# Optimization experiments

Measured on AMD Instinct MI355X. Metric: run time of the kernel, lower is better.

Reference implementation:

```python
import jax, jax.numpy as jnp
import numpy as np

B, C, H, W, S = 32, 512, 32, 32, 4
HW = H * W
OUT = HW // S  # conv1/conv2 out channels = 256
EPS = 1e-5


def setup_inputs() -> dict:
    key = jax.random.key(0)
    ks = jax.random.split(key, 8)
    d = {}
    d["x"] = jax.random.normal(ks[0], (B, C, H, W), jnp.float32)
    # conv1 / bn1 (operate on x_flat with 'channels' = h*w)
    d["w1"] = jax.random.normal(ks[1], (OUT, HW), jnp.float32) * 0.02
    d["b1"] = jnp.zeros((OUT,), jnp.float32)
    d["g1"] = jnp.ones((OUT,), jnp.float32)
    d["be1"] = jnp.zeros((OUT,), jnp.float32)
    d["m1"] = jax.random.normal(ks[2], (OUT,), jnp.float32) * 0.01
    d["v1"] = jnp.ones((OUT,), jnp.float32)
    # conv2 / bn2
    d["w2"] = jax.random.normal(ks[3], (OUT, HW), jnp.float32) * 0.02
    d["b2"] = jnp.zeros((OUT,), jnp.float32)
    d["g2"] = jnp.ones((OUT,), jnp.float32)
    d["be2"] = jnp.zeros((OUT,), jnp.float32)
    d["m2"] = jax.random.normal(ks[4], (OUT,), jnp.float32) * 0.01
    d["v2"] = jnp.ones((OUT,), jnp.float32)
    # conv3 / bn3 (1x1 conv on the real channel dim c)
    d["w3"] = jax.random.normal(ks[5], (C, C), jnp.float32) * 0.02
    d["b3"] = jnp.zeros((C,), jnp.float32)
    d["g3"] = jnp.ones((C,), jnp.float32)
    d["be3"] = jnp.zeros((C,), jnp.float32)
    d["m3"] = jax.random.normal(ks[6], (C,), jnp.float32) * 0.01
    d["v3"] = jnp.ones((C,), jnp.float32)
    # conv4: 1x1 conv mapping 1+2c channels -> 1
    d["w4"] = jax.random.normal(ks[7], (1 + 2 * C,), jnp.float32) * 0.02
    d["b4"] = jnp.zeros((), jnp.float32)
    return d


def _bn1d(t, g, be, m, v):
    # t: [b, o, c]; BatchNorm (eval mode) over channel axis 1
    scale = g / jnp.sqrt(v + EPS)
    return (t - m[:, None]) * scale[:, None] + be[:, None]


def reference(x, w1, b1, g1, be1, m1, v1,
              w2, b2, g2, be2, m2, v2,
              w3, b3, g3, be3, m3, v3,
              w4, b4):
    b, c, h, w = x.shape
    # x_flat: [b, h*w, c] -- conv1/conv2 are 1x1 convs over 'channels' = h*w
    xf = x.reshape(b, c, h * w).transpose(0, 2, 1)
    theta = jax.nn.relu(_bn1d(jnp.einsum('oq,bqc->boc', w1, xf) + b1[:, None],
                              g1, be1, m1, v1))  # [b, OUT, c]
    phi = jax.nn.relu(_bn1d(jnp.einsum('oq,bqc->boc', w2, xf) + b2[:, None],
                            g2, be2, m2, v2))    # [b, OUT, c]
    # per-batch conv2d-as-matmul loop collapses to one batched GEMM:
    # affinity[b, i, j] = sum_k phi[b, k, i] * theta[b, k, j]
    aff = jnp.einsum('bki,bkj->bij', phi, theta)  # [b, c, c]
    # x_embed: 1x1 conv + BN + ReLU + global average pool -> [b, c]
    scale3 = g3 / jnp.sqrt(v3 + EPS)
    xe = jnp.einsum('oc,bchw->bohw', w3, x) + b3[:, None, None]
    xe = jax.nn.relu((xe - m3[:, None, None]) * scale3[:, None, None]
                     + be3[:, None, None])
    xe = xe.mean(axis=(2, 3))  # [b, c]
    # conv4 over y = cat([x_embed, affinity_a, affinity_b], dim=1):
    # affinity_a[b,i,0,p] = aff[b,i,p]; affinity_b[b,i,0,p] = aff[b,p,i]
    logits = (w4[0] * xe
              + jnp.einsum('i,bip->bp', w4[1:1 + c], aff)
              + jnp.einsum('i,bpi->bp', w4[1 + c:], aff)
              + b4)
    a = jax.nn.sigmoid(logits)  # [b, c]
    return x * a[:, :, None, None]
```

## Files before the change

kernel.cpp:

```cpp
#include <hip/hip_runtime.h>
#include <math.h>

#define BB   32
#define CC   512
#define HWW  1024
#define OUTC 256
#define EPSV 1e-5f

typedef __attribute__((ext_vector_type(8))) short bfrag;
typedef __attribute__((ext_vector_type(4))) float f32x4;

__device__ inline unsigned short f2bf(float x){
  unsigned int uu = __float_as_uint(x);
  uu += 0x7fff + ((uu >> 16) & 1);
  return (unsigned short)(uu >> 16);
}
__device__ inline float bf2f(unsigned short h){
  return __uint_as_float(((unsigned int)h) << 16);
}

#define ASYNC16(g, l) \
  __builtin_amdgcn_global_load_lds((const __attribute__((address_space(1))) unsigned int*)(g), \
                                   (__attribute__((address_space(3))) unsigned int*)(l), 16, 0, 0)


__global__ __launch_bounds__(256) void kw_conv(
    const float* __restrict__ w1, const float* __restrict__ w2,
    const float* __restrict__ w3,
    unsigned short* __restrict__ Whi, unsigned short* __restrict__ Wlo,
    unsigned short* __restrict__ W3hi)
{
  int i = blockIdx.x * 256 + threadIdx.x;
  if (i < 512 * 1024) {
    float v = (i < 256 * 1024) ? w1[i] : w2[i - 256 * 1024];
    unsigned short h = f2bf(v);
    Whi[i] = h;
    Wlo[i] = f2bf(v - bf2f(h));
  } else {
    int j = i - 512 * 1024;
    W3hi[j] = f2bf(w3[j]);
  }
}

__global__ __launch_bounds__(256) void k0_x(
    const float* __restrict__ x,
    unsigned short* __restrict__ Xhi, unsigned short* __restrict__ Xlo,
    unsigned short* __restrict__ XThi)
{
  __shared__ float T[64][65];
  const int b = blockIdx.z, c0 = blockIdx.y * 64, p0 = blockIdx.x * 64;
  const int tid = threadIdx.x, tr = tid >> 4, tc4 = (tid & 15) * 4;
  const float* xb = x + (size_t)b * 512 * 1024;
#pragma unroll
  for (int r = 0; r < 4; ++r) {
    int c = c0 + tr + r * 16;
    float4 v = *(const float4*)(xb + (size_t)c * 1024 + p0 + tc4);
    T[tr + r * 16][tc4 + 0] = v.x; T[tr + r * 16][tc4 + 1] = v.y;
    T[tr + r * 16][tc4 + 2] = v.z; T[tr + r * 16][tc4 + 3] = v.w;
    ushort4 h, l;
    h.x = f2bf(v.x); l.x = f2bf(v.x - bf2f(h.x));
    h.y = f2bf(v.y); l.y = f2bf(v.y - bf2f(h.y));
    h.z = f2bf(v.z); l.z = f2bf(v.z - bf2f(h.z));
    h.w = f2bf(v.w); l.w = f2bf(v.w - bf2f(h.w));
    size_t idx = (size_t)b * 524288 + (size_t)c * 1024 + p0 + tc4;
    *(ushort4*)(Xhi + idx) = h;
    *(ushort4*)(Xlo + idx) = l;
  }
  __syncthreads();
#pragma unroll
  for (int r = 0; r < 4; ++r) {
    int pl = tr + r * 16;
    ushort4 h;
    h.x = f2bf(T[tc4 + 0][pl]); h.y = f2bf(T[tc4 + 1][pl]);
    h.z = f2bf(T[tc4 + 2][pl]); h.w = f2bf(T[tc4 + 3][pl]);
    *(ushort4*)(XThi + (size_t)b * 524288 + (size_t)(p0 + pl) * 512 + c0 + tc4) = h;
  }
}

__global__ __launch_bounds__(256) void g1_mfma(
    const unsigned short* __restrict__ Xhi, const unsigned short* __restrict__ Xlo,
    const unsigned short* __restrict__ Whi, const unsigned short* __restrict__ Wlo,
    const float* __restrict__ b1p, const float* __restrict__ g1p,
    const float* __restrict__ be1p, const float* __restrict__ m1p, const float* __restrict__ v1p,
    const float* __restrict__ b2p, const float* __restrict__ g2p,
    const float* __restrict__ be2p, const float* __restrict__ m2p, const float* __restrict__ v2p,
    float* __restrict__ P2)
{
  __shared__ unsigned short sAh[4096], sAl[4096], sBh[4096], sBl[4096];
  const int b  = blockIdx.z;
  const int n0 = blockIdx.x * 128;
  const int c0 = blockIdx.y * 128;
  const int tid = threadIdx.x;
  const int wave = tid >> 6, lane = tid & 63;
  const int lr = lane >> 2, lc = (lane & 3) * 8;
  const int wm = wave & 1, wn = wave >> 1;
  const int fr = lane & 15, fq = lane >> 4;

  const unsigned short* gb; unsigned short* lb;
  if (wave == 0)      { gb = Xhi + (size_t)b * 524288 + (size_t)c0 * 1024; lb = sAh; }
  else if (wave == 1) { gb = Xlo + (size_t)b * 524288 + (size_t)c0 * 1024; lb = sAl; }
  else if (wave == 2) { gb = Whi + (size_t)n0 * 1024; lb = sBh; }
  else                { gb = Wlo + (size_t)n0 * 1024; lb = sBl; }
  gb += (size_t)lr * 1024 + lc;

  f32x4 acc[4][4];
  const f32x4 zz = {0.f, 0.f, 0.f, 0.f};
#pragma unroll
  for (int i = 0; i < 4; ++i)
#pragma unroll
    for (int j = 0; j < 4; ++j) acc[i][j] = zz;

  for (int kq = 0; kq < 1024; kq += 32) {
#pragma unroll
    for (int inst = 0; inst < 8; ++inst)
      ASYNC16(gb + (size_t)inst * 16 * 1024 + kq, lb + inst * 512);
    __syncthreads();
    bfrag ah[4], al[4], bh[4], bl[4];
#pragma unroll
    for (int i = 0; i < 4; ++i) {
      int off = (wm * 64 + i * 16 + fr) * 32 + fq * 8;
      ah[i] = *(const bfrag*)&sAh[off];
      al[i] = *(const bfrag*)&sAl[off];
    }
#pragma unroll
    for (int j = 0; j < 4; ++j) {
      int off = (wn * 64 + j * 16 + fr) * 32 + fq * 8;
      bh[j] = *(const bfrag*)&sBh[off];
      bl[j] = *(const bfrag*)&sBl[off];
    }
#pragma unroll
    for (int i = 0; i < 4; ++i)
#pragma unroll
      for (int j = 0; j < 4; ++j) {
        acc[i][j] = __builtin_amdgcn_mfma_f32_16x16x32_bf16(ah[i], bh[j], acc[i][j], 0, 0, 0);
        acc[i][j] = __builtin_amdgcn_mfma_f32_16x16x32_bf16(ah[i], bl[j], acc[i][j], 0, 0, 0);
        acc[i][j] = __builtin_amdgcn_mfma_f32_16x16x32_bf16(al[i], bh[j], acc[i][j], 0, 0, 0);
      }
    __syncthreads();
  }

#pragma unroll
  for (int j = 0; j < 4; ++j) {
    int co = n0 + wn * 64 + j * 16 + fr;
    float sc, sh;
    if (co < 256) {
      float s = g1p[co] * rsqrtf(v1p[co] + EPSV);
      sc = s; sh = (b1p[co] - m1p[co]) * s + be1p[co];
    } else {
      int q = co - 256;
      float s = g2p[q] * rsqrtf(v2p[q] + EPSV);
      sc = s; sh = (b2p[q] - m2p[q]) * s + be2p[q];
    }
#pragma unroll
    for (int i = 0; i < 4; ++i) {
      int crow = c0 + wm * 64 + i * 16 + fq * 4;
      float* dst = P2 + ((size_t)b * 512 + crow) * 512 + co;
#pragma unroll
      for (int r = 0; r < 4; ++r)
        dst[(size_t)r * 512] = fmaxf(acc[i][j][r] * sc + sh, 0.f);
    }
  }
}

__global__ __launch_bounds__(256) void g2_mfma(
    const unsigned short* __restrict__ W3hi, const unsigned short* __restrict__ XThi,
    const float* __restrict__ b3p, const float* __restrict__ g3p,
    const float* __restrict__ be3p, const float* __restrict__ m3p, const float* __restrict__ v3p,
    float* __restrict__ xe_acc)
{
  __shared__ unsigned short sA[4096], sB[4096];
  const int b  = blockIdx.z;
  const int n0 = blockIdx.x * 128;
  const int m0 = blockIdx.y * 128;
  const int tid = threadIdx.x;
  const int wave = tid >> 6, lane = tid & 63;
  const int lr = lane >> 2, lc = (lane & 3) * 8;
  const int wm = wave & 1, wn = wave >> 1;
  const int fr = lane & 15, fq = lane >> 4;

  const unsigned short* gb; unsigned short* lb;
  if (wave < 2) { gb = W3hi + (size_t)(m0 + wave * 64) * 512; lb = sA + wave * 2048; }
  else { gb = XThi + (size_t)b * 524288 + (size_t)(n0 + (wave - 2) * 64) * 512; lb = sB + (wave - 2) * 2048; }
  gb += (size_t)lr * 512 + lc;

  f32x4 acc[4][4];
  const f32x4 zz = {0.f, 0.f, 0.f, 0.f};
#pragma unroll
  for (int i = 0; i < 4; ++i)
#pragma unroll
    for (int j = 0; j < 4; ++j) acc[i][j] = zz;

  for (int kq = 0; kq < 512; kq += 32) {
#pragma unroll
    for (int inst = 0; inst < 4; ++inst)
      ASYNC16(gb + (size_t)inst * 16 * 512 + kq, lb + inst * 512);
    __syncthreads();
    bfrag af[4], bf[4];
#pragma unroll
    for (int i = 0; i < 4; ++i)
      af[i] = *(const bfrag*)&sA[(wm * 64 + i * 16 + fr) * 32 + fq * 8];
#pragma unroll
    for (int j = 0; j < 4; ++j)
      bf[j] = *(const bfrag*)&sB[(wn * 64 + j * 16 + fr) * 32 + fq * 8];
#pragma unroll
    for (int i = 0; i < 4; ++i)
#pragma unroll
      for (int j = 0; j < 4; ++j)
        acc[i][j] = __builtin_amdgcn_mfma_f32_16x16x32_bf16(af[i], bf[j], acc[i][j], 0, 0, 0);
    __syncthreads();
  }

#pragma unroll
  for (int i = 0; i < 4; ++i) {
#pragma unroll
    for (int r = 0; r < 4; ++r) {
      int o = m0 + wm * 64 + i * 16 + fq * 4 + r;
      float s  = g3p[o] * rsqrtf(v3p[o] + EPSV);
      float sh = (b3p[o] - m3p[o]) * s + be3p[o];
      float v = fmaxf(acc[i][0][r] * s + sh, 0.f) + fmaxf(acc[i][1][r] * s + sh, 0.f)
              + fmaxf(acc[i][2][r] * s + sh, 0.f) + fmaxf(acc[i][3][r] * s + sh, 0.f);
      v += __shfl_xor(v, 1); v += __shfl_xor(v, 2);
      v += __shfl_xor(v, 4); v += __shfl_xor(v, 8);
      if (fr == 0) atomicAdd(&xe_acc[b * 512 + o], v);
    }
  }
}

__global__ __launch_bounds__(256) void k3_dots(
    const float* __restrict__ P2, const float* __restrict__ w4,
    float* __restrict__ u, float* __restrict__ t)
{
  const int b = blockIdx.x, ic = blockIdx.y * 64;
  const int k = threadIdx.x;
  const float* base = P2 + ((size_t)b * 512 + ic) * 512;
  float su = 0.f, st = 0.f;
#pragma unroll 4
  for (int i = 0; i < 64; ++i) {
    float wa = w4[1 + ic + i];
    float wb = w4[513 + ic + i];
    su += wa * base[(size_t)i * 512 + 256 + k];
    st += wb * base[(size_t)i * 512 + k];
  }
  atomicAdd(&u[b * 256 + k], su);
  atomicAdd(&t[b * 256 + k], st);
}

__global__ __launch_bounds__(256) void k4_gate_out(
    const float* __restrict__ P2, const float* __restrict__ u,
    const float* __restrict__ t, const float* __restrict__ xe_acc,
    const float* __restrict__ w4, const float* __restrict__ b4,
    const float* __restrict__ x, float* __restrict__ out)
{
  __shared__ float us[256], ts[256];
  const int b = blockIdx.x;
  us[threadIdx.x] = u[b * 256 + threadIdx.x];
  ts[threadIdx.x] = t[b * 256 + threadIdx.x];
  __syncthreads();
  const int wave = threadIdx.x >> 6, lane = threadIdx.x & 63;
  const int p = blockIdx.y * 4 + wave;
  const float* row = P2 + ((size_t)b * 512 + p) * 512;
  float4 th = *(const float4*)&row[lane * 4];
  float4 ph = *(const float4*)&row[256 + lane * 4];
  int ki = lane * 4;
  float rs = th.x * us[ki] + th.y * us[ki + 1] + th.z * us[ki + 2] + th.w * us[ki + 3]
           + ph.x * ts[ki] + ph.y * ts[ki + 1] + ph.z * ts[ki + 2] + ph.w * ts[ki + 3];
  rs += __shfl_xor(rs, 1);  rs += __shfl_xor(rs, 2);  rs += __shfl_xor(rs, 4);
  rs += __shfl_xor(rs, 8);  rs += __shfl_xor(rs, 16); rs += __shfl_xor(rs, 32);
  float xe = xe_acc[b * 512 + p] * (1.f / 1024.f);
  float logit = w4[0] * xe + rs + b4[0];
  float a = 1.f / (1.f + expf(-logit));
  const float4* xr = (const float4*)(x + ((size_t)b * 512 + p) * 1024);
  float4* orow = (float4*)(out + ((size_t)b * 512 + p) * 1024);
#pragma unroll
  for (int r2 = 0; r2 < 4; ++r2) {
    float4 xv = xr[lane + r2 * 64];
    float4 ov; ov.x = xv.x * a; ov.y = xv.y * a; ov.z = xv.z * a; ov.w = xv.w * a;
    orow[lane + r2 * 64] = ov;
  }
}

__global__ __launch_bounds__(256) void k1_theta_phi(
    const float* __restrict__ x,
    const float* __restrict__ w1, const float* __restrict__ b1,
    const float* __restrict__ g1, const float* __restrict__ be1,
    const float* __restrict__ m1, const float* __restrict__ v1,
    const float* __restrict__ w2, const float* __restrict__ b2,
    const float* __restrict__ g2, const float* __restrict__ be2,
    const float* __restrict__ m2, const float* __restrict__ v2,
    float* __restrict__ P)
{
  __shared__ __align__(16) float Ws[32][68];
  __shared__ __align__(16) float Xs[32][68];
  const int b  = blockIdx.z;
  const int o0 = blockIdx.y * 64;
  const int c0 = blockIdx.x * 64;
  const int tid = threadIdx.x;
  const int tx = tid & 15, ty = tid >> 4;
  const float* __restrict__ Wbase = (o0 < OUTC) ? (w1 + (size_t)o0 * HWW)
                                                : (w2 + (size_t)(o0 - OUTC) * HWW);
  const float* __restrict__ xb = x + (size_t)b * CC * HWW;
  float acc[4][4] = {{0.f}};
  for (int k0 = 0; k0 < HWW; k0 += 32) {
#pragma unroll
    for (int r = 0; r < 2; ++r) {
      int id  = tid + (r << 8);
      int row = id >> 3;
      int cg  = (id & 7) << 2;
      float4 wv = *(const float4*)(Wbase + (size_t)row * HWW + k0 + cg);
      Ws[cg+0][row] = wv.x; Ws[cg+1][row] = wv.y; Ws[cg+2][row] = wv.z; Ws[cg+3][row] = wv.w;
      float4 xv = *(const float4*)(xb + (size_t)(c0 + row) * HWW + k0 + cg);
      Xs[cg+0][row] = xv.x; Xs[cg+1][row] = xv.y; Xs[cg+2][row] = xv.z; Xs[cg+3][row] = xv.w;
    }
    __syncthreads();
#pragma unroll
    for (int k = 0; k < 32; ++k) {
      float4 av = *(const float4*)&Ws[k][ty * 4];
      float4 bv = *(const float4*)&Xs[k][tx * 4];
      acc[0][0] += av.x*bv.x; acc[0][1] += av.x*bv.y; acc[0][2] += av.x*bv.z; acc[0][3] += av.x*bv.w;
      acc[1][0] += av.y*bv.x; acc[1][1] += av.y*bv.y; acc[1][2] += av.y*bv.z; acc[1][3] += av.y*bv.w;
      acc[2][0] += av.z*bv.x; acc[2][1] += av.z*bv.y; acc[2][2] += av.z*bv.z; acc[2][3] += av.z*bv.w;
      acc[3][0] += av.w*bv.x; acc[3][1] += av.w*bv.y; acc[3][2] += av.w*bv.z; acc[3][3] += av.w*bv.w;
    }
    __syncthreads();
  }
  const float *bias, *g, *be, *m, *v; int ob;
  if (o0 < OUTC) { bias = b1; g = g1; be = be1; m = m1; v = v1; ob = o0; }
  else           { bias = b2; g = g2; be = be2; m = m2; v = v2; ob = o0 - OUTC; }
#pragma unroll
  for (int i = 0; i < 4; ++i) {
    int oi = ob + ty * 4 + i;
    float sc = g[oi] * rsqrtf(v[oi] + EPSV);
    float sh = be[oi] - m[oi] * sc;
    float bb = bias[oi];
    float4 ov;
    ov.x = fmaxf((acc[i][0] + bb) * sc + sh, 0.f);
    ov.y = fmaxf((acc[i][1] + bb) * sc + sh, 0.f);
    ov.z = fmaxf((acc[i][2] + bb) * sc + sh, 0.f);
    ov.w = fmaxf((acc[i][3] + bb) * sc + sh, 0.f);
    int oo = o0 + ty * 4 + i;
    *(float4*)(P + ((size_t)b * 512 + oo) * 512 + c0 + tx * 4) = ov;
  }
}

__global__ __launch_bounds__(256) void k2_xe(
    const float* __restrict__ x, const float* __restrict__ w3,
    const float* __restrict__ b3, const float* __restrict__ g3,
    const float* __restrict__ be3, const float* __restrict__ m3,
    const float* __restrict__ v3, float* __restrict__ xe_acc)
{
  __shared__ __align__(16) float As[32][68];
  __shared__ __align__(16) float Bs[32][68];
  const int b  = blockIdx.z;
  const int o0 = blockIdx.y * 64;
  const int p0 = blockIdx.x * 64;
  const int tid = threadIdx.x;
  const int tx = tid & 15, ty = tid >> 4;
  const float* __restrict__ xb = x + (size_t)b * CC * HWW;
  float acc[4][4] = {{0.f}};
  for (int ck = 0; ck < CC; ck += 32) {
#pragma unroll
    for (int r = 0; r < 2; ++r) {
      int id  = tid + (r << 8);
      int row = id >> 3;
      int cg  = (id & 7) << 2;
      float4 wv = *(const float4*)(w3 + (size_t)(o0 + row) * CC + ck + cg);
      As[cg+0][row] = wv.x; As[cg+1][row] = wv.y; As[cg+2][row] = wv.z; As[cg+3][row] = wv.w;
      int brow = id >> 4;
      int pg   = (id & 15) << 2;
      float4 xv = *(const float4*)(xb + (size_t)(ck + brow) * HWW + p0 + pg);
      *(float4*)&Bs[brow][pg] = xv;
    }
    __syncthreads();
#pragma unroll
    for (int k = 0; k < 32; ++k) {
      float4 av = *(const float4*)&As[k][ty * 4];
      float4 bv = *(const float4*)&Bs[k][tx * 4];
      acc[0][0] += av.x*bv.x; acc[0][1] += av.x*bv.y; acc[0][2] += av.x*bv.z; acc[0][3] += av.x*bv.w;
      acc[1][0] += av.y*bv.x; acc[1][1] += av.y*bv.y; acc[1][2] += av.y*bv.z; acc[1][3] += av.y*bv.w;
      acc[2][0] += av.z*bv.x; acc[2][1] += av.z*bv.y; acc[2][2] += av.z*bv.z; acc[2][3] += av.z*bv.w;
      acc[3][0] += av.w*bv.x; acc[3][1] += av.w*bv.y; acc[3][2] += av.w*bv.z; acc[3][3] += av.w*bv.w;
    }
    __syncthreads();
  }
#pragma unroll
  for (int i = 0; i < 4; ++i) {
    int oo = o0 + ty * 4 + i;
    float sc = g3[oo] * rsqrtf(v3[oo] + EPSV);
    float sh = be3[oo] - m3[oo] * sc;
    float bb = b3[oo];
    float ps = fmaxf((acc[i][0] + bb) * sc + sh, 0.f)
             + fmaxf((acc[i][1] + bb) * sc + sh, 0.f)
             + fmaxf((acc[i][2] + bb) * sc + sh, 0.f)
             + fmaxf((acc[i][3] + bb) * sc + sh, 0.f);
    ps += __shfl_xor(ps, 1);
    ps += __shfl_xor(ps, 2);
    ps += __shfl_xor(ps, 4);
    ps += __shfl_xor(ps, 8);
    if (tx == 0) atomicAdd(&xe_acc[b * CC + oo], ps);
  }
}

__global__ __launch_bounds__(256) void k3_ut(
    const float* __restrict__ P, const float* __restrict__ w4,
    float* __restrict__ u, float* __restrict__ t)
{
  const int b = blockIdx.x;
  const int wv = threadIdx.x >> 6, lane = threadIdx.x & 63;
  const int k = blockIdx.y * 4 + wv;
  const float* __restrict__ w4a = w4 + 1;
  const float* __restrict__ w4b = w4 + 1 + CC;
  const float* __restrict__ throw_ = P + ((size_t)b * 512 + k) * 512;
  const float* __restrict__ phrow  = P + ((size_t)b * 512 + 256 + k) * 512;
  float su = 0.f, st = 0.f;
#pragma unroll
  for (int i = lane; i < CC; i += 64) {
    su += w4a[i] * phrow[i];
    st += w4b[i] * throw_[i];
  }
#pragma unroll
  for (int off = 32; off > 0; off >>= 1) {
    su += __shfl_down(su, off);
    st += __shfl_down(st, off);
  }
  if (lane == 0) { u[b * OUTC + k] = su; t[b * OUTC + k] = st; }
}

__global__ __launch_bounds__(256) void k4_gate(
    const float* __restrict__ P, const float* __restrict__ u,
    const float* __restrict__ t, const float* __restrict__ xe_acc,
    const float* __restrict__ w4, const float* __restrict__ b4,
    float* __restrict__ amul)
{
  __shared__ float us[256], ts[256];
  const int b = blockIdx.x;
  const int p = blockIdx.y * 256 + threadIdx.x;
  us[threadIdx.x] = u[b * OUTC + threadIdx.x];
  ts[threadIdx.x] = t[b * OUTC + threadIdx.x];
  __syncthreads();
  const float* __restrict__ theta = P + (size_t)b * 512 * 512;
  const float* __restrict__ phi   = theta + 256 * 512;
  float r = 0.f, s = 0.f;
#pragma unroll 8
  for (int k = 0; k < OUTC; ++k) {
    r += us[k] * theta[(size_t)k * 512 + p];
    s += ts[k] * phi[(size_t)k * 512 + p];
  }
  float xe = xe_acc[b * CC + p] * (1.0f / 1024.0f);
  float logit = w4[0] * xe + r + s + b4[0];
  amul[b * CC + p] = 1.0f / (1.0f + expf(-logit));
}

__global__ __launch_bounds__(256) void k5_out(
    const float* __restrict__ x, const float* __restrict__ amul,
    float* __restrict__ out)
{
  int i = blockIdx.x * 256 + threadIdx.x;
  float4 xv = ((const float4*)x)[i];
  float a = amul[i >> 8];
  float4 ov; ov.x = xv.x * a; ov.y = xv.y * a; ov.z = xv.z * a; ov.w = xv.w * a;
  ((float4*)out)[i] = ov;
}

extern "C" void kernel_launch(void* const* d_in, const int* in_sizes, int n_in,
                              void* d_out, int out_size, void* d_ws, size_t ws_size,
                              hipStream_t stream)
{
  (void)in_sizes; (void)n_in; (void)out_size;
  const float* x   = (const float*)d_in[0];
  const float* w1  = (const float*)d_in[1];
  const float* b1  = (const float*)d_in[2];
  const float* g1  = (const float*)d_in[3];
  const float* be1 = (const float*)d_in[4];
  const float* m1  = (const float*)d_in[5];
  const float* v1  = (const float*)d_in[6];
  const float* w2  = (const float*)d_in[7];
  const float* b2  = (const float*)d_in[8];
  const float* g2  = (const float*)d_in[9];
  const float* be2 = (const float*)d_in[10];
  const float* m2  = (const float*)d_in[11];
  const float* v2  = (const float*)d_in[12];
  const float* w3  = (const float*)d_in[13];
  const float* b3  = (const float*)d_in[14];
  const float* g3  = (const float*)d_in[15];
  const float* be3 = (const float*)d_in[16];
  const float* m3  = (const float*)d_in[17];
  const float* v3  = (const float*)d_in[18];
  const float* w4  = (const float*)d_in[19];
  const float* b4  = (const float*)d_in[20];
  float* out = (float*)d_out;

  if (ws_size >= 136970240ull) {
    float* P2     = (float*)d_ws;
    float* xe_acc = P2 + 8388608;
    float* u      = P2 + 8404992;
    float* t      = P2 + 8413184;
    unsigned short* Xhi  = (unsigned short*)((char*)d_ws + 33685504);
    unsigned short* Xlo  = Xhi + 16777216;
    unsigned short* XThi = Xlo + 16777216;
    unsigned short* Whi  = XThi + 16777216;
    unsigned short* Wlo  = Whi + 524288;
    unsigned short* W3hi = Wlo + 524288;

    hipMemsetAsync(xe_acc, 0, 32768 * sizeof(float), stream);

    kw_conv<<<3072, 256, 0, stream>>>(w1, w2, w3, Whi, Wlo, W3hi);
    k0_x<<<dim3(16, 8, 32), 256, 0, stream>>>(x, Xhi, Xlo, XThi);
    g1_mfma<<<dim3(4, 4, 32), 256, 0, stream>>>(Xhi, Xlo, Whi, Wlo,
        b1, g1, be1, m1, v1, b2, g2, be2, m2, v2, P2);
    g2_mfma<<<dim3(8, 4, 32), 256, 0, stream>>>(W3hi, XThi, b3, g3, be3, m3, v3, xe_acc);
    k3_dots<<<dim3(32, 8), 256, 0, stream>>>(P2, w4, u, t);
    k4_gate_out<<<dim3(32, 128), 256, 0, stream>>>(P2, u, t, xe_acc, w4, b4, x, out);
  } else {
    float* P      = (float*)d_ws;
    float* xe_acc = P + (size_t)BB * 512 * 512;
    float* u      = xe_acc + BB * CC;
    float* t      = u + BB * OUTC;
    float* amul   = t + BB * OUTC;

    hipMemsetAsync(xe_acc, 0, (size_t)BB * CC * sizeof(float), stream);

    dim3 blk(256);
    k1_theta_phi<<<dim3(8, 8, BB), blk, 0, stream>>>(x, w1, b1, g1, be1, m1, v1,
                                                     w2, b2, g2, be2, m2, v2, P);
    k2_xe<<<dim3(16, 8, BB), blk, 0, stream>>>(x, w3, b3, g3, be3, m3, v3, xe_acc);
    k3_ut<<<dim3(BB, 64), blk, 0, stream>>>(P, w4, u, t);
    k4_gate<<<dim3(BB, 2), blk, 0, stream>>>(P, u, t, xe_acc, w4, b4, amul);
    k5_out<<<dim3((BB * CC * HWW / 4) / 256), blk, 0, stream>>>(x, amul, out);
  }
}
```

Before: 291.4 us.

## Fuse conv4 dot products into GEMM epilogue, merge prep kernels, swizzle LDS

The weighted reductions over theta/phi rows (the old k3_dots kernel) now run inside the g1_mfma epilogue. Each block combines its ReLU outputs with w4, reduces across lanes with shuffles and atomically adds into u/t, so the separate pass that re-read the large P2 buffer is gone. The weight-conversion and x-conversion kernels are merged into one launch, with an extra z-slice doing the weight work. g1 blocks are remapped with an XCD-aware index so neighbouring tiles share L2, and both GEMMs use an XOR swizzle on LDS chunk placement to reduce bank conflicts. The costs are more atomics and a longer epilogue in the GEMM.

```diff
diff --git a/kernel.cpp b/kernel.cpp
--- a/kernel.cpp
+++ b/kernel.cpp
@@ -24,29 +24,30 @@
                                    (__attribute__((address_space(3))) unsigned int*)(l), 16, 0, 0)
 
 
-__global__ __launch_bounds__(256) void kw_conv(
+__global__ __launch_bounds__(256) void prep(
+    const float* __restrict__ x,
     const float* __restrict__ w1, const float* __restrict__ w2,
     const float* __restrict__ w3,
+    unsigned short* __restrict__ Xhi, unsigned short* __restrict__ Xlo,
+    unsigned short* __restrict__ XThi,
     unsigned short* __restrict__ Whi, unsigned short* __restrict__ Wlo,
     unsigned short* __restrict__ W3hi)
 {
-  int i = blockIdx.x * 256 + threadIdx.x;
-  if (i < 512 * 1024) {
-    float v = (i < 256 * 1024) ? w1[i] : w2[i - 256 * 1024];
-    unsigned short h = f2bf(v);
-    Whi[i] = h;
-    Wlo[i] = f2bf(v - bf2f(h));
-  } else {
-    int j = i - 512 * 1024;
-    W3hi[j] = f2bf(w3[j]);
-  }
-}
-
-__global__ __launch_bounds__(256) void k0_x(
-    const float* __restrict__ x,
-    unsigned short* __restrict__ Xhi, unsigned short* __restrict__ Xlo,
-    unsigned short* __restrict__ XThi)
-{
+  if (blockIdx.z == 32) {
+    int worker = (blockIdx.y * 16 + blockIdx.x) * 256 + threadIdx.x;
+    for (int i = worker; i < 786432; i += 32768) {
+      if (i < 524288) {
+        float v = (i < 262144) ? w1[i] : w2[i - 262144];
+        unsigned short h = f2bf(v);
+        Whi[i] = h;
+        Wlo[i] = f2bf(v - bf2f(h));
+      } else {
+        int j = i - 524288;
+        W3hi[j] = f2bf(w3[j]);
+      }
+    }
+    return;
+  }
   __shared__ float T[64][65];
   const int b = blockIdx.z, c0 = blockIdx.y * 64, p0 = blockIdx.x * 64;
   const int tid = threadIdx.x, tr = tid >> 4, tc4 = (tid & 15) * 4;
@@ -84,24 +85,30 @@
     const float* __restrict__ be1p, const float* __restrict__ m1p, const float* __restrict__ v1p,
     const float* __restrict__ b2p, const float* __restrict__ g2p,
     const float* __restrict__ be2p, const float* __restrict__ m2p, const float* __restrict__ v2p,
-    float* __restrict__ P2)
+    const float* __restrict__ w4,
+    float* __restrict__ P2, float* __restrict__ u, float* __restrict__ t)
 {
   __shared__ unsigned short sAh[4096], sAl[4096], sBh[4096], sBl[4096];
-  const int b  = blockIdx.z;
-  const int n0 = blockIdx.x * 128;
-  const int c0 = blockIdx.y * 128;
-  const int tid = threadIdx.x;
+  const int f    = blockIdx.x;
+  const int xcd  = f & 7;
+  const int n0   = ((f >> 3) & 3) * 128;
+  const int g    = ((f >> 5) << 3) | xcd;
+  const int b    = g >> 2;
+  const int c0   = (g & 3) * 128;
+  const int tid  = threadIdx.x;
   const int wave = tid >> 6, lane = tid & 63;
-  const int lr = lane >> 2, lc = (lane & 3) * 8;
+  const int lr = lane >> 2;
+  const int lcs = ((lane & 3) ^ (lr & 3)) * 8;
   const int wm = wave & 1, wn = wave >> 1;
   const int fr = lane & 15, fq = lane >> 4;
+  const int fsw = (fq ^ (fr & 3)) * 8;
 
   const unsigned short* gb; unsigned short* lb;
   if (wave == 0)      { gb = Xhi + (size_t)b * 524288 + (size_t)c0 * 1024; lb = sAh; }
   else if (wave == 1) { gb = Xlo + (size_t)b * 524288 + (size_t)c0 * 1024; lb = sAl; }
   else if (wave == 2) { gb = Whi + (size_t)n0 * 1024; lb = sBh; }
   else                { gb = Wlo + (size_t)n0 * 1024; lb = sBl; }
-  gb += (size_t)lr * 1024 + lc;
+  gb += (size_t)lr * 1024 + lcs;
 
   f32x4 acc[4][4];
   const f32x4 zz = {0.f, 0.f, 0.f, 0.f};
@@ -118,13 +125,13 @@
     bfrag ah[4], al[4], bh[4], bl[4];
 #pragma unroll
     for (int i = 0; i < 4; ++i) {
-      int off = (wm * 64 + i * 16 + fr) * 32 + fq * 8;
+      int off = (wm * 64 + i * 16 + fr) * 32 + fsw;
       ah[i] = *(const bfrag*)&sAh[off];
       al[i] = *(const bfrag*)&sAl[off];
     }
 #pragma unroll
     for (int j = 0; j < 4; ++j) {
-      int off = (wn * 64 + j * 16 + fr) * 32 + fq * 8;
+      int off = (wn * 64 + j * 16 + fr) * 32 + fsw;
       bh[j] = *(const bfrag*)&sBh[off];
       bl[j] = *(const bfrag*)&sBl[off];
     }
@@ -139,26 +146,40 @@
     __syncthreads();
   }
 
+  const float *bias, *gg, *bes, *mm, *vv_; int cof;
+  if (n0 < 256) { bias = b1p; gg = g1p; bes = be1p; mm = m1p; vv_ = v1p; cof = 0; }
+  else          { bias = b2p; gg = g2p; bes = be2p; mm = m2p; vv_ = v2p; cof = 256; }
+  const float* wsel = (n0 < 256) ? (w4 + 513) : (w4 + 1);
+  float* dsel = (n0 < 256) ? (t + b * 256) : (u + b * 256);
+  const int cobase = ((n0 < 256) ? n0 : n0 - 256) + wn * 64;
+  float wt[4][4];
+#pragma unroll
+  for (int i = 0; i < 4; ++i)
+#pragma unroll
+    for (int r = 0; r < 4; ++r)
+      wt[i][r] = wsel[c0 + wm * 64 + i * 16 + fq * 4 + r];
+
 #pragma unroll
   for (int j = 0; j < 4; ++j) {
     int co = n0 + wn * 64 + j * 16 + fr;
-    float sc, sh;
-    if (co < 256) {
-      float s = g1p[co] * rsqrtf(v1p[co] + EPSV);
-      sc = s; sh = (b1p[co] - m1p[co]) * s + be1p[co];
-    } else {
-      int q = co - 256;
-      float s = g2p[q] * rsqrtf(v2p[q] + EPSV);
-      sc = s; sh = (b2p[q] - m2p[q]) * s + be2p[q];
-    }
+    int q = co - cof;
+    float s  = gg[q] * rsqrtf(vv_[q] + EPSV);
+    float sh = (bias[q] - mm[q]) * s + bes[q];
+    float psum = 0.f;
 #pragma unroll
     for (int i = 0; i < 4; ++i) {
       int crow = c0 + wm * 64 + i * 16 + fq * 4;
       float* dst = P2 + ((size_t)b * 512 + crow) * 512 + co;
 #pragma unroll
-      for (int r = 0; r < 4; ++r)
-        dst[(size_t)r * 512] = fmaxf(acc[i][j][r] * sc + sh, 0.f);
-    }
+      for (int r = 0; r < 4; ++r) {
+        float val = fmaxf(acc[i][j][r] * s + sh, 0.f);
+        dst[(size_t)r * 512] = val;
+        psum += wt[i][r] * val;
+      }
+    }
+    psum += __shfl_xor(psum, 16);
+    psum += __shfl_xor(psum, 32);
+    if (fq == 0) atomicAdd(&dsel[cobase + j * 16 + fr], psum);
   }
 }
 
@@ -174,14 +195,16 @@
   const int m0 = blockIdx.y * 128;
   const int tid = threadIdx.x;
   const int wave = tid >> 6, lane = tid & 63;
-  const int lr = lane >> 2, lc = (lane & 3) * 8;
+  const int lr = lane >> 2;
+  const int lcs = ((lane & 3) ^ (lr & 3)) * 8;
   const int wm = wave & 1, wn = wave >> 1;
   const int fr = lane & 15, fq = lane >> 4;
+  const int fsw = (fq ^ (fr & 3)) * 8;
 
   const unsigned short* gb; unsigned short* lb;
   if (wave < 2) { gb = W3hi + (size_t)(m0 + wave * 64) * 512; lb = sA + wave * 2048; }
   else { gb = XThi + (size_t)b * 524288 + (size_t)(n0 + (wave - 2) * 64) * 512; lb = sB + (wave - 2) * 2048; }
-  gb += (size_t)lr * 512 + lc;
+  gb += (size_t)lr * 512 + lcs;
 
   f32x4 acc[4][4];
   const f32x4 zz = {0.f, 0.f, 0.f, 0.f};
@@ -198,10 +221,10 @@
     bfrag af[4], bf[4];
 #pragma unroll
     for (int i = 0; i < 4; ++i)
-      af[i] = *(const bfrag*)&sA[(wm * 64 + i * 16 + fr) * 32 + fq * 8];
+      af[i] = *(const bfrag*)&sA[(wm * 64 + i * 16 + fr) * 32 + fsw];
 #pragma unroll
     for (int j = 0; j < 4; ++j)
-      bf[j] = *(const bfrag*)&sB[(wn * 64 + j * 16 + fr) * 32 + fq * 8];
+      bf[j] = *(const bfrag*)&sB[(wn * 64 + j * 16 + fr) * 32 + fsw];
 #pragma unroll
     for (int i = 0; i < 4; ++i)
 #pragma unroll
@@ -224,25 +247,6 @@
       if (fr == 0) atomicAdd(&xe_acc[b * 512 + o], v);
     }
   }
-}
-
-__global__ __launch_bounds__(256) void k3_dots(
-    const float* __restrict__ P2, const float* __restrict__ w4,
-    float* __restrict__ u, float* __restrict__ t)
-{
-  const int b = blockIdx.x, ic = blockIdx.y * 64;
-  const int k = threadIdx.x;
-  const float* base = P2 + ((size_t)b * 512 + ic) * 512;
-  float su = 0.f, st = 0.f;
-#pragma unroll 4
-  for (int i = 0; i < 64; ++i) {
-    float wa = w4[1 + ic + i];
-    float wb = w4[513 + ic + i];
-    su += wa * base[(size_t)i * 512 + 256 + k];
-    st += wb * base[(size_t)i * 512 + k];
-  }
-  atomicAdd(&u[b * 256 + k], su);
-  atomicAdd(&t[b * 256 + k], st);
 }
 
 __global__ __launch_bounds__(256) void k4_gate_out(
@@ -503,12 +507,11 @@
 
     hipMemsetAsync(xe_acc, 0, 32768 * sizeof(float), stream);
 
-    kw_conv<<<3072, 256, 0, stream>>>(w1, w2, w3, Whi, Wlo, W3hi);
-    k0_x<<<dim3(16, 8, 32), 256, 0, stream>>>(x, Xhi, Xlo, XThi);
-    g1_mfma<<<dim3(4, 4, 32), 256, 0, stream>>>(Xhi, Xlo, Whi, Wlo,
-        b1, g1, be1, m1, v1, b2, g2, be2, m2, v2, P2);
+    prep<<<dim3(16, 8, 33), 256, 0, stream>>>(x, w1, w2, w3, Xhi, Xlo, XThi,
+                                              Whi, Wlo, W3hi);
+    g1_mfma<<<dim3(512), 256, 0, stream>>>(Xhi, Xlo, Whi, Wlo,
+        b1, g1, be1, m1, v1, b2, g2, be2, m2, v2, w4, P2, u, t);
     g2_mfma<<<dim3(8, 4, 32), 256, 0, stream>>>(W3hi, XThi, b3, g3, be3, m3, v3, xe_acc);
-    k3_dots<<<dim3(32, 8), 256, 0, stream>>>(P2, w4, u, t);
     k4_gate_out<<<dim3(32, 128), 256, 0, stream>>>(P2, u, t, xe_acc, w4, b4, x, out);
   } else {
     float* P      = (float*)d_ws;
```

After: 291.8 us. Within noise of the previous version (+0.1%).
